# Performance work log

Hardware: AMD Instinct MI355X
Metric: run time of the kernel (lower is better)

## Reference

```python
import jax, jax.numpy as jnp
import numpy as np

D_MODEL = 1024
N_HEAD = 16


def setup_inputs() -> dict:
    key = jax.random.key(0)
    ks = jax.random.split(key, 12)
    B, T, D = 2, 2048, D_MODEL
    s = 1.0 / np.sqrt(D)
    return {
        "q": jax.random.normal(ks[0], (B, T, D), jnp.float32),
        "k": jax.random.normal(ks[1], (B, T, D), jnp.float32),
        "v": jax.random.normal(ks[2], (B, T, D), jnp.float32),
        "w_q": jax.random.normal(ks[3], (D, D), jnp.float32) * s,
        "b_q": jnp.zeros((D,), jnp.float32),
        "w_k": jax.random.normal(ks[4], (D, D), jnp.float32) * s,
        "b_k": jnp.zeros((D,), jnp.float32),
        "w_v": jax.random.normal(ks[5], (D, D), jnp.float32) * s,
        "b_v": jnp.zeros((D,), jnp.float32),
        "w_o": jax.random.normal(ks[6], (D, D), jnp.float32) * s,
        "b_o": jnp.zeros((D,), jnp.float32),
    }


def reference(q, k, v, w_q, b_q, w_k, b_k, w_v, b_v, w_o, b_o):
    B, T, D = q.shape
    H = N_HEAD
    nd = D // H  # head dim
    # projections (weights stored as [in, out])
    qh = (q @ w_q + b_q).reshape(B, T, H, nd).transpose(0, 2, 1, 3)  # [b,h,t,nd]
    kh = (k @ w_k + b_k).reshape(B, T, H, nd).transpose(0, 2, 1, 3)
    vh = (v @ w_v + b_v).reshape(B, T, H, nd).transpose(0, 2, 1, 3)
    score = jnp.einsum('bhqd,bhkd->bhqk', qh, kh) / jnp.sqrt(jnp.float32(nd))
    causal = jnp.tril(jnp.ones((T, T), dtype=bool))  # [tq, tk]
    score = jnp.where(causal, score, -jnp.inf)
    # NOTE: original module uses nn.Softmax(dim=-2), i.e. softmax over the
    # QUERY axis. Faithful to the source.
    attn = jax.nn.softmax(score, axis=-2)
    out = jnp.einsum('bhqk,bhkd->bhqd', attn, vh)  # [b,h,t,nd]
    out = out.transpose(0, 2, 1, 3).reshape(B, T, D)
    return out @ w_o + b_o
```

## Files before the change

### kernel.cpp

```cpp
#include <hip/hip_runtime.h>
#include <hip/hip_bf16.h>
#include <cstdint>
#include <cstddef>

#define D_MODEL 1024
#define NHEAD   16
#define HDIM    64
#define BB      2
#define TT      2048
#define MM      (BB*TT)
#define BHN     (BB*NHEAD)

typedef __attribute__((ext_vector_type(8))) __bf16 bf16x8;
typedef __attribute__((ext_vector_type(4))) float  f32x4;
typedef __attribute__((ext_vector_type(8))) unsigned short u16x8;
typedef __attribute__((ext_vector_type(4))) unsigned short u16x4;

__device__ __forceinline__ unsigned short f2b(float f){
  __bf16 b = (__bf16)f;
  return __builtin_bit_cast(unsigned short, b);
}
__device__ __forceinline__ float b2f(unsigned short u){
  unsigned int x = ((unsigned int)u) << 16;
  return __builtin_bit_cast(float, x);
}

__device__ __forceinline__ f32x4 mfma16(bf16x8 a, bf16x8 b, f32x4 c){
  return __builtin_amdgcn_mfma_f32_16x16x32_bf16(a, b, c, 0, 0, 0);
}

__device__ __forceinline__ void gload16(const void* g, void* lds){
  __builtin_amdgcn_global_load_lds((const __attribute__((address_space(1))) void*)g,
                                   (__attribute__((address_space(3))) void*)lds, 16, 0, 0);
}

#define SWZ(byteoff, row) ((byteoff) ^ (((row)&7)<<4))

__global__ void cvt_bf16_kernel(const float* __restrict__ q, const float* __restrict__ k,
                                const float* __restrict__ v,
                                unsigned short* __restrict__ Xq, unsigned short* __restrict__ Xk,
                                unsigned short* __restrict__ Xv){
  const int z = blockIdx.y;
  const float* x = z==0 ? q : z==1 ? k : v;
  unsigned short* y = z==0 ? Xq : z==1 ? Xk : Xv;
  size_t i = (size_t)blockIdx.x*blockDim.x + threadIdx.x;
  const float4* p = (const float4*)(x + i*8);
  float4 a = p[0], b = p[1];
  u16x8 o;
  o[0]=f2b(a.x); o[1]=f2b(a.y); o[2]=f2b(a.z); o[3]=f2b(a.w);
  o[4]=f2b(b.x); o[5]=f2b(b.y); o[6]=f2b(b.z); o[7]=f2b(b.w);
  *(u16x8*)(y + i*8) = o;
}

__global__ void transpose_w_kernel(const float* __restrict__ W0, const float* __restrict__ W1,
                                   const float* __restrict__ W2, const float* __restrict__ W3,
                                   unsigned short* __restrict__ T0, unsigned short* __restrict__ T1,
                                   unsigned short* __restrict__ T2, unsigned short* __restrict__ T3){
  __shared__ float tile[32][33];
  const int z = blockIdx.z;
  const float* W = z==0 ? W0 : z==1 ? W1 : z==2 ? W2 : W3;
  unsigned short* Wt = z==0 ? T0 : z==1 ? T1 : z==2 ? T2 : T3;
  int tx = threadIdx.x, ty = threadIdx.y;
  int x0 = blockIdx.x*32, y0 = blockIdx.y*32;
  #pragma unroll
  for (int i=0;i<4;i++)
    tile[ty + i*8][tx] = W[(size_t)(y0 + ty + i*8)*D_MODEL + x0 + tx];
  __syncthreads();
  #pragma unroll
  for (int i=0;i<4;i++)
    Wt[(size_t)(x0 + ty + i*8)*D_MODEL + y0 + tx] = f2b(tile[tx][ty + i*8]);
}

__device__ __forceinline__ void gemm_body(const unsigned short* __restrict__ A,
                                          const unsigned short* __restrict__ Bt,
                                          const float* __restrict__ bias,
                                          void* __restrict__ Cout, const int mode,
                                          const int m0, const int n0)
{
  constexpr int K = D_MODEL, N = D_MODEL;
  __shared__ unsigned short As[128*64];
  __shared__ unsigned short Bs[128*64];
  const int t = threadIdx.x, lane = t&63, w = t>>6;
  const int wr = w>>1, wc = w&1, lr = lane&15, lg = lane>>4;
  const int osrc = (lane&7) ^ (lane>>3);
  f32x4 acc[4][4] = {};
  for (int k0 = 0; k0 < K; k0 += 64){
    __syncthreads();
    #pragma unroll
    for (int g=0; g<4; g++){
      int reg = w*4 + g;
      int r = reg*8 + (lane>>3);
      gload16(A  + (size_t)(m0+r)*K + k0 + osrc*8, (char*)As + reg*1024);
      gload16(Bt + (size_t)(n0+r)*K + k0 + osrc*8, (char*)Bs + reg*1024);
    }
    __syncthreads();
    #pragma unroll
    for (int ks=0; ks<2; ks++){
      bf16x8 af[4], bfv[4];
      #pragma unroll
      for (int mi=0;mi<4;mi++){
        int r = wr*64 + mi*16 + lr;
        af[mi] = *(const bf16x8*)((const char*)As + r*128 + (((ks*4+lg) ^ (r&7))*16));
      }
      #pragma unroll
      for (int ni=0;ni<4;ni++){
        int r = wc*64 + ni*16 + lr;
        bfv[ni] = *(const bf16x8*)((const char*)Bs + r*128 + (((ks*4+lg) ^ (r&7))*16));
      }
      #pragma unroll
      for (int mi=0;mi<4;mi++)
        #pragma unroll
        for (int ni=0;ni<4;ni++)
          acc[mi][ni] = mfma16(af[mi], bfv[ni], acc[mi][ni]);
    }
  }
  #pragma unroll
  for (int mi=0;mi<4;mi++){
    #pragma unroll
    for (int ni=0;ni<4;ni++){
      int n = n0 + wc*64 + ni*16 + lr;
      int mbase = m0 + wr*64 + mi*16 + lg*4;
      float bv = bias[n];
      if (mode == 0){
        unsigned short* Cb = (unsigned short*)Cout;
        #pragma unroll
        for (int r=0;r<4;r++) Cb[(size_t)(mbase+r)*N + n] = f2b(acc[mi][ni][r] + bv);
      } else {
        unsigned short* Vt = (unsigned short*)Cout;
        int h = n >> 6, d = n & 63;
        int b = mbase >> 11;
        int tq = mbase & (TT-1);
        u16x4 vv;
        #pragma unroll
        for (int r=0;r<4;r++) vv[r] = f2b(acc[mi][ni][r] + bv);
        *(u16x4*)(Vt + ((size_t)((b*NHEAD + h)*HDIM + d))*TT + tq) = vv;
      }
    }
  }
}

__launch_bounds__(256)
__global__ void proj_gemm_kernel(const unsigned short* __restrict__ Xq,
                                 const unsigned short* __restrict__ Xk,
                                 const unsigned short* __restrict__ Xv,
                                 const unsigned short* __restrict__ Wtq,
                                 const unsigned short* __restrict__ Wtk,
                                 const unsigned short* __restrict__ Wtv,
                                 const float* __restrict__ b_q, const float* __restrict__ b_k,
                                 const float* __restrict__ b_v,
                                 unsigned short* __restrict__ Qb, unsigned short* __restrict__ Kb,
                                 unsigned short* __restrict__ Vt)
{
  const int id = blockIdx.x;
  const int xcd = id & 7, r2 = id >> 3;
  const int n = r2 & 7, mz = r2 >> 3;
  const int m = (mz & 3)*8 + xcd, z = mz >> 2;
  const unsigned short* A  = z==0 ? Xq : z==1 ? Xk : Xv;
  const unsigned short* Bt = z==0 ? Wtq : z==1 ? Wtk : Wtv;
  const float* bias = z==0 ? b_q : z==1 ? b_k : b_v;
  void* C = z==0 ? (void*)Qb : z==1 ? (void*)Kb : (void*)Vt;
  gemm_body(A, Bt, bias, C, z==2 ? 1 : 0, m*128, n*128);
}

__launch_bounds__(256)
__global__ void out_gemm_kernel(const unsigned short* __restrict__ Ob,
                                const unsigned short* __restrict__ Wto,
                                const float* __restrict__ b_o, float* __restrict__ out)
{
  constexpr int K = D_MODEL, N = D_MODEL;
  __shared__ unsigned short As[64*64];
  __shared__ unsigned short Bs[128*64];
  const int id = blockIdx.x;
  const int xcd = id & 7, r2 = id >> 3;
  const int n0 = (r2 & 7)*128, m0 = ((r2 >> 3)*8 + xcd)*64;
  const int t = threadIdx.x, lane = t&63, w = t>>6;
  const int wr = w>>1, wc = w&1, lr = lane&15, lg = lane>>4;
  const int osrc = (lane&7) ^ (lane>>3);
  f32x4 acc[2][4] = {};
  for (int k0 = 0; k0 < K; k0 += 64){
    __syncthreads();
    #pragma unroll
    for (int g=0; g<2; g++){
      int reg = w*2 + g;
      int r = reg*8 + (lane>>3);
      gload16(Ob + (size_t)(m0+r)*K + k0 + osrc*8, (char*)As + reg*1024);
    }
    #pragma unroll
    for (int g=0; g<4; g++){
      int reg = w*4 + g;
      int r = reg*8 + (lane>>3);
      gload16(Wto + (size_t)(n0+r)*K + k0 + osrc*8, (char*)Bs + reg*1024);
    }
    __syncthreads();
    #pragma unroll
    for (int ks=0; ks<2; ks++){
      bf16x8 af[2], bfv[4];
      #pragma unroll
      for (int mi=0;mi<2;mi++){
        int r = wr*32 + mi*16 + lr;
        af[mi] = *(const bf16x8*)((const char*)As + r*128 + (((ks*4+lg) ^ (r&7))*16));
      }
      #pragma unroll
      for (int ni=0;ni<4;ni++){
        int r = wc*64 + ni*16 + lr;
        bfv[ni] = *(const bf16x8*)((const char*)Bs + r*128 + (((ks*4+lg) ^ (r&7))*16));
      }
      #pragma unroll
      for (int mi=0;mi<2;mi++)
        #pragma unroll
        for (int ni=0;ni<4;ni++)
          acc[mi][ni] = mfma16(af[mi], bfv[ni], acc[mi][ni]);
    }
  }
  #pragma unroll
  for (int mi=0;mi<2;mi++){
    #pragma unroll
    for (int ni=0;ni<4;ni++){
      int n = n0 + wc*64 + ni*16 + lr;
      int mbase = m0 + wr*32 + mi*16 + lg*4;
      float bv = b_o[n];
      #pragma unroll
      for (int r=0;r<4;r++) out[(size_t)(mbase+r)*N + n] = acc[mi][ni][r] + bv;
    }
  }
}

__launch_bounds__(256)
__global__ void col_stats_kernel(const unsigned short* __restrict__ Qb,
                                 const unsigned short* __restrict__ Kb,
                                 float* __restrict__ partialS)
{
  __shared__ unsigned short Ks[128*64];
  __shared__ unsigned short Qs[64*64];
  const int t = threadIdx.x, lane = t&63, w = t>>6;
  const int id = blockIdx.x;
  const int bh = id & 31, pair = id >> 5;
  const int kb_ = pair & 15, qc = pair >> 4;
  const int b = bh >> 4, h = bh & 15;
  const int k0 = kb_ * 128;
  const int lr = lane&15, lg = lane>>4;
  const int osrc = (lane&7) ^ (lane>>3);
  #pragma unroll
  for (int g=0; g<4; g++){
    int reg = w*4 + g;
    int r = reg*8 + (lane>>3);
    gload16(Kb + ((size_t)(b*TT + k0 + r))*D_MODEL + h*64 + osrc*8, (char*)Ks + reg*1024);
  }
  __syncthreads();
  bf16x8 bk[2][2];
  #pragma unroll
  for (int kb=0;kb<2;kb++)
    #pragma unroll
    for (int ks=0;ks<2;ks++){
      int r = w*32 + kb*16 + lr;
      bk[kb][ks] = *(const bf16x8*)((const char*)Ks + r*128 + (((ks*4+lg) ^ (r&7))*16));
    }
  f32x4 sacc[2] = {};
  const int qstart = (k0 > qc*256) ? k0 : qc*256;
  const int qend   = (qc+1)*256;
  for (int qt = qstart; qt < qend; qt += 64){
    __syncthreads();
    #pragma unroll
    for (int g=0; g<2; g++){
      int reg = w*2 + g;
      int r = reg*8 + (lane>>3);
      gload16(Qb + ((size_t)(b*TT + qt + r))*D_MODEL + h*64 + osrc*8, (char*)Qs + reg*1024);
    }
    __syncthreads();
    const bool interior = (qt >= k0 + 128);
    #pragma unroll
    for (int qb=0;qb<4;qb++){
      bf16x8 aq[2];
      #pragma unroll
      for (int ks=0;ks<2;ks++){
        int r = qb*16 + lr;
        aq[ks] = *(const bf16x8*)((const char*)Qs + r*128 + (((ks*4+lg) ^ (r&7))*16));
      }
      f32x4 sf[2] = {};
      #pragma unroll
      for (int ks=0;ks<2;ks++)
        #pragma unroll
        for (int kb=0;kb<2;kb++)
          sf[kb] = mfma16(aq[ks], bk[kb][ks], sf[kb]);
      #pragma unroll
      for (int kb=0;kb<2;kb++){
        int col = k0 + w*32 + kb*16 + lr;
        #pragma unroll
        for (int r=0;r<4;r++){
          float e = __expf(sf[kb][r] * 0.125f);
          if (!interior){
            int qg = qt + qb*16 + lg*4 + r;
            e = (qg >= col) ? e : 0.f;
          }
          sacc[kb][r] += e;
        }
      }
    }
  }
  #pragma unroll
  for (int kb=0;kb<2;kb++){
    float s = sacc[kb][0] + sacc[kb][1] + sacc[kb][2] + sacc[kb][3];
    s += __shfl_xor(s, 16);
    s += __shfl_xor(s, 32);
    if (lg == 0){
      int col = k0 + w*32 + kb*16 + lr;
      partialS[((size_t)qc*BHN + bh)*TT + col] = s;
    }
  }
}

__global__ void col_combine_kernel(const float* __restrict__ partialS, float* __restrict__ colS){
  int i = blockIdx.x*256 + threadIdx.x;
  float s = 0.f;
  #pragma unroll
  for (int qc=0;qc<8;qc++) s += partialS[(size_t)qc*BHN*TT + i];
  colS[i] = 1.0f / s;
}

__global__ void vscale_kernel(unsigned short* __restrict__ Vt, const float* __restrict__ colS){
  size_t c = (size_t)blockIdx.x*256 + threadIdx.x;
  int t0  = (int)(c & 255) * 8;
  int row = (int)(c >> 8);
  int bh  = row >> 6;
  u16x8 v = *(u16x8*)(Vt + (size_t)row*TT + t0);
  const float4* cs = (const float4*)(colS + (size_t)bh*TT + t0);
  float4 s0 = cs[0], s1 = cs[1];
  v[0]=f2b(b2f(v[0])*s0.x); v[1]=f2b(b2f(v[1])*s0.y);
  v[2]=f2b(b2f(v[2])*s0.z); v[3]=f2b(b2f(v[3])*s0.w);
  v[4]=f2b(b2f(v[4])*s1.x); v[5]=f2b(b2f(v[5])*s1.y);
  v[6]=f2b(b2f(v[6])*s1.z); v[7]=f2b(b2f(v[7])*s1.w);
  *(u16x8*)(Vt + (size_t)row*TT + t0) = v;
}

__launch_bounds__(256)
__global__ void attn_out_kernel(const unsigned short* __restrict__ Qb,
                                const unsigned short* __restrict__ Kb,
                                const unsigned short* __restrict__ Vt,
                                unsigned short* __restrict__ O)
{
  __shared__ unsigned short Qs[64*64];
  __shared__ unsigned short Ks2[64*64];
  __shared__ unsigned short Vs[64*64];
  __shared__ unsigned short Ps[64*64];
  const int t = threadIdx.x, lane=t&63, w=t>>6;
  const int id = blockIdx.x;
  const int bh = id & 31;
  const int qi = 31 - (id >> 5);
  const int b = bh>>4, h = bh&15;
  const int q0 = qi*64;
  const int lr = lane&15, lg = lane>>4;
  const int osrc = (lane&7) ^ (lane>>3);
  #pragma unroll
  for (int g=0; g<2; g++){
    int reg = w*2 + g;
    int r = reg*8 + (lane>>3);
    gload16(Qb + ((size_t)(b*TT + q0 + r))*D_MODEL + h*64 + osrc*8, (char*)Qs + reg*1024);
  }
  __syncthreads();
  bf16x8 aq[2];
  #pragma unroll
  for (int ks=0;ks<2;ks++){
    int r = w*16 + lr;
    aq[ks] = *(const bf16x8*)((const char*)Qs + r*128 + (((ks*4+lg) ^ (r&7))*16));
  }
  f32x4 oacc[4] = {};
  const int nkt = qi + 1;
  for (int kt=0; kt<nkt; kt++){
    int k0 = kt*64;
    __syncthreads();
    #pragma unroll
    for (int g=0; g<2; g++){
      int reg = w*2 + g;
      int r = reg*8 + (lane>>3);
      gload16(Kb + ((size_t)(b*TT + k0 + r))*D_MODEL + h*64 + osrc*8, (char*)Ks2 + reg*1024);
      gload16(Vt + ((size_t)(bh*HDIM + r))*TT + k0 + osrc*8, (char*)Vs + reg*1024);
    }
    __syncthreads();
    f32x4 sf[4] = {};
    #pragma unroll
    for (int ks=0;ks<2;ks++)
      #pragma unroll
      for (int kb=0;kb<4;kb++){
        int r = kb*16 + lr;
        bf16x8 bk = *(const bf16x8*)((const char*)Ks2 + r*128 + (((ks*4+lg) ^ (r&7))*16));
        sf[kb] = mfma16(bk, aq[ks], sf[kb]);
      }
    const bool boundary = (kt == qi);
    const int prow = w*16 + lr;
    #pragma unroll
    for (int kb=0;kb<4;kb++){
      u16x4 vv;
      #pragma unroll
      for (int r=0;r<4;r++){
        float pv = __expf(sf[kb][r]*0.125f);
        if (boundary){
          int kg = k0 + kb*16 + lg*4 + r;
          int qg = q0 + prow;
          pv = (qg >= kg) ? pv : 0.f;
        }
        vv[r] = f2b(pv);
      }
      *(u16x4*)((char*)Ps + SWZ(prow*128 + kb*32 + lg*8, prow)) = vv;
    }
    #pragma unroll
    for (int ks=0;ks<2;ks++){
      bf16x8 pa = *(const bf16x8*)((const char*)Ps + prow*128 + (((ks*4+lg) ^ (prow&7))*16));
      #pragma unroll
      for (int db=0;db<4;db++){
        int r = db*16 + lr;
        bf16x8 bv = *(const bf16x8*)((const char*)Vs + r*128 + (((ks*4+lg) ^ (r&7))*16));
        oacc[db] = mfma16(pa, bv, oacc[db]);
      }
    }
  }
  #pragma unroll
  for (int db=0;db<4;db++){
    int qg = q0 + w*16 + lg*4;
    int d  = db*16 + lr;
    #pragma unroll
    for (int r=0;r<4;r++)
      O[((size_t)(b*TT + qg + r))*D_MODEL + h*64 + d] = f2b(oacc[db][r]);
  }
}

extern "C" void kernel_launch(void* const* d_in, const int* in_sizes, int n_in,
                              void* d_out, int out_size, void* d_ws, size_t ws_size,
                              hipStream_t stream)
{
  (void)in_sizes; (void)n_in; (void)out_size; (void)ws_size;
  const float* q   = (const float*)d_in[0];
  const float* k   = (const float*)d_in[1];
  const float* v   = (const float*)d_in[2];
  const float* w_q = (const float*)d_in[3];
  const float* b_q = (const float*)d_in[4];
  const float* w_k = (const float*)d_in[5];
  const float* b_k = (const float*)d_in[6];
  const float* w_v = (const float*)d_in[7];
  const float* b_v = (const float*)d_in[8];
  const float* w_o = (const float*)d_in[9];
  const float* b_o = (const float*)d_in[10];

  char* p = (char*)d_ws;
  auto carve = [&](size_t bytes)->char* {
    char* r = p; p += (bytes + 255) & ~(size_t)255; return r;
  };
  unsigned short* Xq  = (unsigned short*)carve((size_t)MM*D_MODEL*2);
  unsigned short* Xk  = (unsigned short*)carve((size_t)MM*D_MODEL*2);
  unsigned short* Xv  = (unsigned short*)carve((size_t)MM*D_MODEL*2);
  unsigned short* Wtq = (unsigned short*)carve((size_t)D_MODEL*D_MODEL*2);
  unsigned short* Wtk = (unsigned short*)carve((size_t)D_MODEL*D_MODEL*2);
  unsigned short* Wtv = (unsigned short*)carve((size_t)D_MODEL*D_MODEL*2);
  unsigned short* Wto = (unsigned short*)carve((size_t)D_MODEL*D_MODEL*2);
  unsigned short* Qb  = (unsigned short*)carve((size_t)MM*D_MODEL*2);
  unsigned short* Kb  = (unsigned short*)carve((size_t)MM*D_MODEL*2);
  unsigned short* Vt  = (unsigned short*)carve((size_t)MM*D_MODEL*2);
  unsigned short* Ob  = (unsigned short*)carve((size_t)MM*D_MODEL*2);
  float* partialS = (float*)carve((size_t)8*BHN*TT*4);
  float* colS     = (float*)carve((size_t)BHN*TT*4);

  cvt_bf16_kernel<<<dim3((MM*D_MODEL/8)/256, 3), 256, 0, stream>>>(q, k, v, Xq, Xk, Xv);

  dim3 tgrid(32,32,4), tblk(32,8);
  transpose_w_kernel<<<tgrid, tblk, 0, stream>>>(w_q, w_k, w_v, w_o, Wtq, Wtk, Wtv, Wto);

  proj_gemm_kernel<<<dim3(768), 256, 0, stream>>>(Xq, Xk, Xv, Wtq, Wtk, Wtv,
                                                  b_q, b_k, b_v, Qb, Kb, Vt);

  col_stats_kernel<<<dim3(8*16*BHN), 256, 0, stream>>>(Qb, Kb, partialS);
  col_combine_kernel<<<dim3(BHN*TT/256), 256, 0, stream>>>(partialS, colS);

  vscale_kernel<<<dim3((BHN*HDIM*TT/8)/256), 256, 0, stream>>>(Vt, colS);

  attn_out_kernel<<<dim3((TT/64)*BHN), 256, 0, stream>>>(Qb, Kb, Vt, Ob);

  out_gemm_kernel<<<dim3(512), 256, 0, stream>>>(Ob, Wto, b_o, (float*)d_out);
}
```

Before: 143.9 us.

## Double-buffer LDS tiles to overlap global loads with MFMA across all kernels

Adds ping-pong LDS buffers to the projection GEMM, output GEMM, column-stats and attention kernels so the next tile's global-to-LDS load is issued before computing on the current tile. This cuts the per-iteration syncs from two to one. The GEMMs also shrink the K-step from 64 to 32 with a new 4-chunk XOR swizzle, keeping LDS use about the same but doubling loop iterations. The cost is more shared memory in the attention kernels, which may lower occupancy. There is also a risk that the asynchronous LDS loads are not properly waited on before the single barrier.

```diff
diff --git a/kernel.cpp b/kernel.cpp
--- a/kernel.cpp
+++ b/kernel.cpp
@@ -33,8 +33,6 @@
   __builtin_amdgcn_global_load_lds((const __attribute__((address_space(1))) void*)g,
                                    (__attribute__((address_space(3))) void*)lds, 16, 0, 0);
 }
-
-#define SWZ(byteoff, row) ((byteoff) ^ (((row)&7)<<4))
 
 __global__ void cvt_bf16_kernel(const float* __restrict__ q, const float* __restrict__ k,
                                 const float* __restrict__ v,
@@ -78,42 +76,52 @@
                                           const int m0, const int n0)
 {
   constexpr int K = D_MODEL, N = D_MODEL;
-  __shared__ unsigned short As[128*64];
-  __shared__ unsigned short Bs[128*64];
+  __shared__ unsigned short As[2][128*32];
+  __shared__ unsigned short Bs[2][128*32];
   const int t = threadIdx.x, lane = t&63, w = t>>6;
   const int wr = w>>1, wc = w&1, lr = lane&15, lg = lane>>4;
-  const int osrc = (lane&7) ^ (lane>>3);
+  const int srow = lane>>2;
+  const int schunk = (lane&3) ^ ((lane>>3)&3);
+  const int crd = lg ^ ((lr>>1)&3);
   f32x4 acc[4][4] = {};
-  for (int k0 = 0; k0 < K; k0 += 64){
+
+  auto stage = [&](int buf, int k0){
+    #pragma unroll
+    for (int g=0; g<2; g++){
+      int reg = w*2 + g;
+      int r = reg*16 + srow;
+      gload16(A  + (size_t)(m0+r)*K + k0 + schunk*8, (char*)As[buf] + reg*1024);
+      gload16(Bt + (size_t)(n0+r)*K + k0 + schunk*8, (char*)Bs[buf] + reg*1024);
+    }
+  };
+
+  stage(0, 0);
+  __syncthreads();
+  int buf = 0;
+  for (int ks = 0; ks < 32; ++ks){
+    if (ks < 31) stage(buf^1, (ks+1)*32);
+    const char* bufA = (const char*)As[buf];
+    const char* bufB = (const char*)Bs[buf];
+    bf16x8 af[4], bfv[4];
+    #pragma unroll
+    for (int mi=0;mi<4;mi++){
+      int r = wr*64 + mi*16 + lr;
+      af[mi] = *(const bf16x8*)(bufA + r*64 + crd*16);
+    }
+    #pragma unroll
+    for (int ni=0;ni<4;ni++){
+      int r = wc*64 + ni*16 + lr;
+      bfv[ni] = *(const bf16x8*)(bufB + r*64 + crd*16);
+    }
+    #pragma unroll
+    for (int mi=0;mi<4;mi++)
+      #pragma unroll
+      for (int ni=0;ni<4;ni++)
+        acc[mi][ni] = mfma16(af[mi], bfv[ni], acc[mi][ni]);
     __syncthreads();
-    #pragma unroll
-    for (int g=0; g<4; g++){
-      int reg = w*4 + g;
-      int r = reg*8 + (lane>>3);
-      gload16(A  + (size_t)(m0+r)*K + k0 + osrc*8, (char*)As + reg*1024);
-      gload16(Bt + (size_t)(n0+r)*K + k0 + osrc*8, (char*)Bs + reg*1024);
-    }
-    __syncthreads();
-    #pragma unroll
-    for (int ks=0; ks<2; ks++){
-      bf16x8 af[4], bfv[4];
-      #pragma unroll
-      for (int mi=0;mi<4;mi++){
-        int r = wr*64 + mi*16 + lr;
-        af[mi] = *(const bf16x8*)((const char*)As + r*128 + (((ks*4+lg) ^ (r&7))*16));
-      }
-      #pragma unroll
-      for (int ni=0;ni<4;ni++){
-        int r = wc*64 + ni*16 + lr;
-        bfv[ni] = *(const bf16x8*)((const char*)Bs + r*128 + (((ks*4+lg) ^ (r&7))*16));
-      }
-      #pragma unroll
-      for (int mi=0;mi<4;mi++)
-        #pragma unroll
-        for (int ni=0;ni<4;ni++)
-          acc[mi][ni] = mfma16(af[mi], bfv[ni], acc[mi][ni]);
-    }
-  }
+    buf ^= 1;
+  }
+
   #pragma unroll
   for (int mi=0;mi<4;mi++){
     #pragma unroll
@@ -168,50 +176,56 @@
                                 const float* __restrict__ b_o, float* __restrict__ out)
 {
   constexpr int K = D_MODEL, N = D_MODEL;
-  __shared__ unsigned short As[64*64];
-  __shared__ unsigned short Bs[128*64];
+  __shared__ unsigned short As[2][64*32];
+  __shared__ unsigned short Bs[2][128*32];
   const int id = blockIdx.x;
   const int xcd = id & 7, r2 = id >> 3;
   const int n0 = (r2 & 7)*128, m0 = ((r2 >> 3)*8 + xcd)*64;
   const int t = threadIdx.x, lane = t&63, w = t>>6;
   const int wr = w>>1, wc = w&1, lr = lane&15, lg = lane>>4;
-  const int osrc = (lane&7) ^ (lane>>3);
+  const int srow = lane>>2;
+  const int schunk = (lane&3) ^ ((lane>>3)&3);
+  const int crd = lg ^ ((lr>>1)&3);
   f32x4 acc[2][4] = {};
-  for (int k0 = 0; k0 < K; k0 += 64){
-    __syncthreads();
+
+  auto stage = [&](int buf, int k0){
+    { int r = w*16 + srow;
+      gload16(Ob + (size_t)(m0+r)*K + k0 + schunk*8, (char*)As[buf] + w*1024); }
     #pragma unroll
     for (int g=0; g<2; g++){
       int reg = w*2 + g;
-      int r = reg*8 + (lane>>3);
-      gload16(Ob + (size_t)(m0+r)*K + k0 + osrc*8, (char*)As + reg*1024);
-    }
-    #pragma unroll
-    for (int g=0; g<4; g++){
-      int reg = w*4 + g;
-      int r = reg*8 + (lane>>3);
-      gload16(Wto + (size_t)(n0+r)*K + k0 + osrc*8, (char*)Bs + reg*1024);
-    }
+      int r = reg*16 + srow;
+      gload16(Wto + (size_t)(n0+r)*K + k0 + schunk*8, (char*)Bs[buf] + reg*1024);
+    }
+  };
+
+  stage(0, 0);
+  __syncthreads();
+  int buf = 0;
+  for (int ks = 0; ks < 32; ++ks){
+    if (ks < 31) stage(buf^1, (ks+1)*32);
+    const char* bufA = (const char*)As[buf];
+    const char* bufB = (const char*)Bs[buf];
+    bf16x8 af[2], bfv[4];
+    #pragma unroll
+    for (int mi=0;mi<2;mi++){
+      int r = wr*32 + mi*16 + lr;
+      af[mi] = *(const bf16x8*)(bufA + r*64 + crd*16);
+    }
+    #pragma unroll
+    for (int ni=0;ni<4;ni++){
+      int r = wc*64 + ni*16 + lr;
+      bfv[ni] = *(const bf16x8*)(bufB + r*64 + crd*16);
+    }
+    #pragma unroll
+    for (int mi=0;mi<2;mi++)
+      #pragma unroll
+      for (int ni=0;ni<4;ni++)
+        acc[mi][ni] = mfma16(af[mi], bfv[ni], acc[mi][ni]);
     __syncthreads();
-    #pragma unroll
-    for (int ks=0; ks<2; ks++){
-      bf16x8 af[2], bfv[4];
-      #pragma unroll
-      for (int mi=0;mi<2;mi++){
-        int r = wr*32 + mi*16 + lr;
-        af[mi] = *(const bf16x8*)((const char*)As + r*128 + (((ks*4+lg) ^ (r&7))*16));
-      }
-      #pragma unroll
-      for (int ni=0;ni<4;ni++){
-        int r = wc*64 + ni*16 + lr;
-        bfv[ni] = *(const bf16x8*)((const char*)Bs + r*128 + (((ks*4+lg) ^ (r&7))*16));
-      }
-      #pragma unroll
-      for (int mi=0;mi<2;mi++)
-        #pragma unroll
-        for (int ni=0;ni<4;ni++)
-          acc[mi][ni] = mfma16(af[mi], bfv[ni], acc[mi][ni]);
-    }
-  }
+    buf ^= 1;
+  }
+
   #pragma unroll
   for (int mi=0;mi<2;mi++){
     #pragma unroll
@@ -231,7 +245,7 @@
                                  float* __restrict__ partialS)
 {
   __shared__ unsigned short Ks[128*64];
-  __shared__ unsigned short Qs[64*64];
+  __shared__ unsigned short Qs[2][64*64];
   const int t = threadIdx.x, lane = t&63, w = t>>6;
   const int id = blockIdx.x;
   const int bh = id & 31, pair = id >> 5;
@@ -240,13 +254,29 @@
   const int k0 = kb_ * 128;
   const int lr = lane&15, lg = lane>>4;
   const int osrc = (lane&7) ^ (lane>>3);
+
+  auto stageQ = [&](int buf, int qt){
+    #pragma unroll
+    for (int g=0; g<2; g++){
+      int reg = w*2 + g;
+      int r = reg*8 + (lane>>3);
+      gload16(Qb + ((size_t)(b*TT + qt + r))*D_MODEL + h*64 + osrc*8,
+              (char*)Qs[buf] + reg*1024);
+    }
+  };
+
+  const int qstart = (k0 > qc*256) ? k0 : qc*256;
+  const int qend   = (qc+1)*256;
+
   #pragma unroll
   for (int g=0; g<4; g++){
     int reg = w*4 + g;
     int r = reg*8 + (lane>>3);
     gload16(Kb + ((size_t)(b*TT + k0 + r))*D_MODEL + h*64 + osrc*8, (char*)Ks + reg*1024);
   }
+  if (qstart < qend) stageQ(0, qstart);
   __syncthreads();
+
   bf16x8 bk[2][2];
   #pragma unroll
   for (int kb=0;kb<2;kb++)
@@ -256,17 +286,10 @@
       bk[kb][ks] = *(const bf16x8*)((const char*)Ks + r*128 + (((ks*4+lg) ^ (r&7))*16));
     }
   f32x4 sacc[2] = {};
-  const int qstart = (k0 > qc*256) ? k0 : qc*256;
-  const int qend   = (qc+1)*256;
+  int buf = 0;
   for (int qt = qstart; qt < qend; qt += 64){
-    __syncthreads();
-    #pragma unroll
-    for (int g=0; g<2; g++){
-      int reg = w*2 + g;
-      int r = reg*8 + (lane>>3);
-      gload16(Qb + ((size_t)(b*TT + qt + r))*D_MODEL + h*64 + osrc*8, (char*)Qs + reg*1024);
-    }
-    __syncthreads();
+    if (qt + 64 < qend) stageQ(buf^1, qt+64);
+    const char* bufQ = (const char*)Qs[buf];
     const bool interior = (qt >= k0 + 128);
     #pragma unroll
     for (int qb=0;qb<4;qb++){
@@ -274,7 +297,7 @@
       #pragma unroll
       for (int ks=0;ks<2;ks++){
         int r = qb*16 + lr;
-        aq[ks] = *(const bf16x8*)((const char*)Qs + r*128 + (((ks*4+lg) ^ (r&7))*16));
+        aq[ks] = *(const bf16x8*)(bufQ + r*128 + (((ks*4+lg) ^ (r&7))*16));
       }
       f32x4 sf[2] = {};
       #pragma unroll
@@ -296,6 +319,8 @@
         }
       }
     }
+    __syncthreads();
+    buf ^= 1;
   }
   #pragma unroll
   for (int kb=0;kb<2;kb++){
@@ -339,8 +364,8 @@
                                 unsigned short* __restrict__ O)
 {
   __shared__ unsigned short Qs[64*64];
-  __shared__ unsigned short Ks2[64*64];
-  __shared__ unsigned short Vs[64*64];
+  __shared__ unsigned short Ks2[2][64*64];
+  __shared__ unsigned short Vs[2][64*64];
   __shared__ unsigned short Ps[64*64];
   const int t = threadIdx.x, lane=t&63, w=t>>6;
   const int id = blockIdx.x;
@@ -350,13 +375,28 @@
   const int q0 = qi*64;
   const int lr = lane&15, lg = lane>>4;
   const int osrc = (lane&7) ^ (lane>>3);
+
+  auto stageKV = [&](int buf, int k0){
+    #pragma unroll
+    for (int g=0; g<2; g++){
+      int reg = w*2 + g;
+      int r = reg*8 + (lane>>3);
+      gload16(Kb + ((size_t)(b*TT + k0 + r))*D_MODEL + h*64 + osrc*8,
+              (char*)Ks2[buf] + reg*1024);
+      gload16(Vt + ((size_t)(bh*HDIM + r))*TT + k0 + osrc*8,
+              (char*)Vs[buf] + reg*1024);
+    }
+  };
+
   #pragma unroll
   for (int g=0; g<2; g++){
     int reg = w*2 + g;
     int r = reg*8 + (lane>>3);
     gload16(Qb + ((size_t)(b*TT + q0 + r))*D_MODEL + h*64 + osrc*8, (char*)Qs + reg*1024);
   }
+  stageKV(0, 0);
   __syncthreads();
+
   bf16x8 aq[2];
   #pragma unroll
   for (int ks=0;ks<2;ks++){
@@ -365,24 +405,19 @@
   }
   f32x4 oacc[4] = {};
   const int nkt = qi + 1;
+  int buf = 0;
   for (int kt=0; kt<nkt; kt++){
     int k0 = kt*64;
-    __syncthreads();
-    #pragma unroll
-    for (int g=0; g<2; g++){
-      int reg = w*2 + g;
-      int r = reg*8 + (lane>>3);
-      gload16(Kb + ((size_t)(b*TT + k0 + r))*D_MODEL + h*64 + osrc*8, (char*)Ks2 + reg*1024);
-      gload16(Vt + ((size_t)(bh*HDIM + r))*TT + k0 + osrc*8, (char*)Vs + reg*1024);
-    }
-    __syncthreads();
+    if (kt+1 < nkt) stageKV(buf^1, k0+64);
+    const char* bufK = (const char*)Ks2[buf];
+    const char* bufV = (const char*)Vs[buf];
     f32x4 sf[4] = {};
     #pragma unroll
     for (int ks=0;ks<2;ks++)
       #pragma unroll
       for (int kb=0;kb<4;kb++){
         int r = kb*16 + lr;
-        bf16x8 bk = *(const bf16x8*)((const char*)Ks2 + r*128 + (((ks*4+lg) ^ (r&7))*16));
+        bf16x8 bk = *(const bf16x8*)(bufK + r*128 + (((ks*4+lg) ^ (r&7))*16));
         sf[kb] = mfma16(bk, aq[ks], sf[kb]);
       }
     const bool boundary = (kt == qi);
@@ -400,7 +435,7 @@
         }
         vv[r] = f2b(pv);
       }
-      *(u16x4*)((char*)Ps + SWZ(prow*128 + kb*32 + lg*8, prow)) = vv;
+      *(u16x4*)((char*)Ps + ((prow*128 + kb*32 + lg*8) ^ ((prow&7)<<4))) = vv;
     }
     #pragma unroll
     for (int ks=0;ks<2;ks++){
@@ -408,10 +443,12 @@
       #pragma unroll
       for (int db=0;db<4;db++){
         int r = db*16 + lr;
-        bf16x8 bv = *(const bf16x8*)((const char*)Vs + r*128 + (((ks*4+lg) ^ (r&7))*16));
+        bf16x8 bv = *(const bf16x8*)(bufV + r*128 + (((ks*4+lg) ^ (r&7))*16));
         oacc[db] = mfma16(pa, bv, oacc[db]);
       }
     }
+    __syncthreads();
+    buf ^= 1;
   }
   #pragma unroll
   for (int db=0;db<4;db++){
```

After: 140.7 us. 2.3% less time.
